# Kernel optimization log

Measured on AMD Instinct MI355X. Metric: run time of the kernel, lower is better.

The kernel has to match this reference:

```python
import jax, jax.numpy as jnp
import numpy as np

N, E, F_IN, HID = 50000, 800000, 64, 64
RADIAL = 16  # 4 coordinate channels -> 4x4 gram matrix


def _l2norm(x, eps=1e-12):
    # F.normalize(x, dim=-1, p=2)
    n = jnp.linalg.norm(x, axis=-1, keepdims=True)
    return x / jnp.maximum(n, eps)


def setup_inputs() -> dict:
    key = jax.random.key(0)
    ks = jax.random.split(key, 14)

    def lin(k, i, o, scale=None):
        s = (1.0 / np.sqrt(i)) if scale is None else scale
        return (jax.random.normal(k, (i, o), jnp.float32) * s).astype(jnp.float32)

    return dict(
        h=jax.random.normal(ks[0], (N, F_IN), jnp.float32),
        Z=jax.random.normal(ks[1], (N, 4, 3), jnp.float32),
        row=jax.random.randint(ks[2], (E,), 0, N),
        col=jax.random.randint(ks[3], (E,), 0, N),
        # edge_mlp: Linear(2*F_IN+16, HID) -> ReLU -> Linear(HID, HID) -> ReLU
        We1=lin(ks[4], 2 * F_IN + RADIAL, HID), be1=jnp.zeros((HID,), jnp.float32),
        We2=lin(ks[5], HID, HID), be2=jnp.zeros((HID,), jnp.float32),
        # node_mlp: Linear(HID+F_IN+HID, HID) -> ReLU -> Linear(HID, F_IN)
        Wn1=lin(ks[6], HID + F_IN + HID, HID), bn1=jnp.zeros((HID,), jnp.float32),
        Wn2=lin(ks[7], HID, F_IN), bn2=jnp.zeros((F_IN,), jnp.float32),
        # coord_mlp: Linear(HID, HID) -> ReLU -> Linear(HID, 1, bias=False, xavier gain 1e-3)
        Wc1=lin(ks[8], HID, HID), bc1=jnp.zeros((HID,), jnp.float32),
        Wc2=lin(ks[9], HID, 1, scale=0.001),
        # coord_mlp_vel: Linear(F_IN, HID) -> ReLU -> Linear(HID, 1)
        Wv1=lin(ks[10], F_IN, HID), bv1=jnp.zeros((HID,), jnp.float32),
        Wv2=lin(ks[11], HID, 1), bv2=jnp.zeros((1,), jnp.float32),
    )


def reference(h, Z, row, col, We1, be1, We2, be2, Wn1, bn1, Wn2, bn2,
              Wc1, bc1, Wc2, Wv1, bv1, Wv2, bv2):
    n = h.shape[0]
    # ---- coord2radial ----
    coord_diff = Z[row] - Z[col]                                 # [E,4,3]
    gram = jnp.einsum('ejt,ekt->ejk', coord_diff, coord_diff)    # [E,4,4]
    radial = _l2norm(gram.reshape(gram.shape[0], -1))            # [E,16]
    # ---- edge model ----
    e_in = jnp.concatenate([h[row], h[col], radial], axis=1)     # [E,144]
    edge_feat = jax.nn.relu(jax.nn.relu(e_in @ We1 + be1) @ We2 + be2)  # [E,HID]
    # ---- coord model (segment-mean over receiving node `row`) ----
    phi = jax.nn.relu(edge_feat @ Wc1 + bc1) @ Wc2               # [E,1]
    trans = coord_diff * phi[:, :, None]                         # [E,4,3]
    seg = jax.ops.segment_sum(trans, row, num_segments=n)        # [N,4,3]
    ones_e = jnp.ones((row.shape[0],), trans.dtype)
    cnt_row = jnp.maximum(jax.ops.segment_sum(ones_e, row, num_segments=n), 1.0)
    f = seg / cnt_row[:, None, None]                             # coords_weight = 1.0
    Z_new = Z + f                                                # [N,4,3]
    # ---- node model ----
    agg = jax.ops.segment_sum(edge_feat, row, num_segments=n)    # [N,HID]
    cnt_col = jnp.maximum(jax.ops.segment_sum(ones_e, col, num_segments=n), 1.0)
    others = jax.ops.segment_sum(edge_feat, col, num_segments=n) / cnt_col[:, None]
    n_in = jnp.concatenate([others, h, agg], axis=1)             # [N, HID+F_IN+HID]
    h_new = h + (jax.nn.relu(n_in @ Wn1 + bn1) @ Wn2 + bn2)      # recurrent
    # ---- Isolated update: x = Z[:,0], v = Z[:,1], force = f[:,0] ----
    scale = jax.nn.relu(h_new @ Wv1 + bv1) @ Wv2 + bv2           # [N,1]
    v_new = scale * Z[:, 1] + f[:, 0]                            # [N,3]
    x_new = Z[:, 0] + v_new                                      # [N,3]
    return (h_new, Z_new, x_new, v_new)
```

## Files before the change

kernel.cpp:

```cpp
#include <hip/hip_runtime.h>
#include <stdint.h>


__device__ __forceinline__ uint32_t bf16round(float x) {
    uint32_t u = __float_as_uint(x);
    return (u + 0x7fffu + ((u >> 16) & 1u)) >> 16;
}
__device__ __forceinline__ uint32_t packbf(float a, float b) {
    return bf16round(a) | (bf16round(b) << 16);
}
__device__ __forceinline__ float bflo(uint32_t u) { return __uint_as_float(u << 16); }
__device__ __forceinline__ float bfhi(uint32_t u) { return __uint_as_float(u & 0xffff0000u); }
__device__ __forceinline__ float bfu(ushort u) { return __uint_as_float(((uint32_t)u) << 16); }

typedef __attribute__((ext_vector_type(8))) short short8;
typedef __attribute__((ext_vector_type(4))) float f32x4;

__device__ __forceinline__ int wave_incl_scan(int x) {
    int lane = threadIdx.x & 63;
    #pragma unroll
    for (int off = 1; off < 64; off <<= 1) {
        int y = __shfl_up(x, off, 64);
        if (lane >= off) x += y;
    }
    return x;
}

__global__ __launch_bounds__(256) void hist_rank(
    const int* __restrict__ row, const int* __restrict__ col,
    int* __restrict__ cntR, int* __restrict__ cntC,
    int* __restrict__ rank_r, int* __restrict__ rank_c, int E)
{
    int i = blockIdx.x * blockDim.x + threadIdx.x;
    int stride = gridDim.x * blockDim.x;
    for (; i < E; i += stride) {
        rank_r[i] = atomicAdd(&cntR[row[i]], 1);
        rank_c[i] = atomicAdd(&cntC[col[i]], 1);
    }
}

__global__ __launch_bounds__(1024) void scan_block(
    const int* __restrict__ srcR, const int* __restrict__ srcC,
    int* __restrict__ dstR, int* __restrict__ dstC,
    int* __restrict__ bsumR, int* __restrict__ bsumC, int N)
{
    const int* src = blockIdx.y ? srcC : srcR;
    int* dst  = blockIdx.y ? dstC : dstR;
    int* bsum = blockIdx.y ? bsumC : bsumR;
    __shared__ int s[17];
    int tid = threadIdx.x, lane = tid & 63, wid = tid >> 6;
    int i = blockIdx.x * 1024 + tid;
    int x = (i < N) ? src[i] : 0;
    int incl = wave_incl_scan(x);
    if (lane == 63) s[wid] = incl;
    __syncthreads();
    if (wid == 0) {
        int t = (lane < 16) ? s[lane] : 0;
        int sc = t;
        #pragma unroll
        for (int off = 1; off < 16; off <<= 1) {
            int y = __shfl_up(sc, off, 64);
            if (lane >= off) sc += y;
        }
        if (lane < 16) s[lane] = sc - t;
        if (lane == 15) s[16] = sc;
    }
    __syncthreads();
    if (i < N) dst[i] = s[wid] + incl - x;
    if (tid == 0) bsum[blockIdx.x] = s[16];
}

__global__ __launch_bounds__(64) void scan_totals(
    int* __restrict__ bsumR, int* __restrict__ bsumC,
    int* __restrict__ dstR, int* __restrict__ dstC, int nblk, int N)
{
    int lane = threadIdx.x;
    for (int which = 0; which < 2; which++) {
        int* bs = which ? bsumC : bsumR;
        int* dst = which ? dstC : dstR;
        int running = 0;
        for (int base = 0; base < nblk; base += 64) {
            int idx = base + lane;
            int x = (idx < nblk) ? bs[idx] : 0;
            int incl = wave_incl_scan(x);
            if (idx < nblk) bs[idx] = running + incl - x;
            running += __shfl(incl, 63, 64);
        }
        if (lane == 0) dst[N] = running;
    }
}

__global__ __launch_bounds__(1024) void scan_add(
    int* __restrict__ dstR, int* __restrict__ dstC,
    const int* __restrict__ bsumR, const int* __restrict__ bsumC, int N)
{
    int* dst = blockIdx.y ? dstC : dstR;
    const int* bsum = blockIdx.y ? bsumC : bsumR;
    int i = blockIdx.x * 1024 + threadIdx.x;
    if (i < N) dst[i] += bsum[blockIdx.x];
}

__global__ __launch_bounds__(256) void perm_build(
    const int* __restrict__ row, const int* __restrict__ col,
    const int* __restrict__ rowptr, const int* __restrict__ colptr,
    const int* __restrict__ rank_r, const int* __restrict__ rank_c,
    int* __restrict__ rs_row, int* __restrict__ rs_col, int* __restrict__ rs_pc, int E)
{
    int i = blockIdx.x * blockDim.x + threadIdx.x;
    int stride = gridDim.x * blockDim.x;
    for (; i < E; i += stride) {
        int r = row[i], c = col[i];
        int pr = rowptr[r] + rank_r[i];
        int pc = colptr[c] + rank_c[i];
        rs_row[pr] = r;
        rs_col[pr] = c;
        rs_pc[pr]  = pc;
    }
}

__global__ __launch_bounds__(256) void precompute_xrowcol(
    const float* __restrict__ h, const float* __restrict__ We1,
    const float* __restrict__ be1,
    ushort* __restrict__ Xrow, ushort* __restrict__ Xcol,
    ushort* __restrict__ hbf, int N)
{
    __shared__ uint32_t sWa[32 * 64];
    __shared__ uint32_t sWb[32 * 64];
    __shared__ float sbe1[64];
    int tid = threadIdx.x;
    for (int idx = tid; idx < 32 * 64; idx += 256) {
        int p = idx >> 6, o = idx & 63;
        sWa[idx] = packbf(We1[(2 * p) * 64 + o],      We1[(2 * p + 1) * 64 + o]);
        sWb[idx] = packbf(We1[(64 + 2 * p) * 64 + o], We1[(64 + 2 * p + 1) * 64 + o]);
    }
    if (tid < 64) sbe1[tid] = be1[tid];
    __syncthreads();

    int lane = tid & 63;
    int wv = blockIdx.x * 4 + (tid >> 6);
    int nw = gridDim.x * 4;
    for (int n0 = wv; n0 < N; n0 += nw) {
        int n = __builtin_amdgcn_readfirstlane(n0);
        const float* hn = h + (size_t)n * 64;
        float acc1 = sbe1[lane], acc2 = 0.f;
        #pragma unroll 8
        for (int p = 0; p < 32; p++) {
            float a0 = hn[2 * p], a1 = hn[2 * p + 1];
            uint32_t wa = sWa[p * 64 + lane];
            uint32_t wb = sWb[p * 64 + lane];
            acc1 += a0 * bflo(wa) + a1 * bfhi(wa);
            acc2 += a0 * bflo(wb) + a1 * bfhi(wb);
        }
        Xrow[(size_t)n * 64 + lane] = (ushort)bf16round(acc1);
        Xcol[(size_t)n * 64 + lane] = (ushort)bf16round(acc2);
        hbf[(size_t)n * 64 + lane]  = (ushort)bf16round(hn[lane]);
    }
}

__global__ __launch_bounds__(256) void edge_kernel(
    const float* __restrict__ Z,
    const int* __restrict__ rs_row, const int* __restrict__ rs_col,
    const int* __restrict__ rs_pc,
    const ushort* __restrict__ Xrow, const ushort* __restrict__ Xcol,
    const float* __restrict__ We1, const float* __restrict__ We2, const float* __restrict__ be2,
    const float* __restrict__ Wc1, const float* __restrict__ bc1, const float* __restrict__ Wc2,
    ushort* __restrict__ ef_col,
    float* __restrict__ aggF, float* __restrict__ segF, int E)
{
    __shared__ ushort radT[4][16 * 32];
    __shared__ ushort h1T[4][16 * 72];
    __shared__ ushort efT[4][16 * 72];
    __shared__ ushort xrT[4][16 * 72];
    __shared__ float  cdT[4][16 * 12];
    __shared__ float  phiT[4][16];

    int tid   = threadIdx.x;
    int lane  = tid & 63;
    int wslot = tid >> 6;
    int l16   = lane & 15;
    int quad  = lane >> 4;

    short8 w1r[4], w2f0[4], w2f1[4], w3f0[4], w3f1[4];
    float be2v[4], bc1v[4], wc2v[4];
    #pragma unroll
    for (int nt = 0; nt < 4; nt++) {
        int n = nt * 16 + l16;
        #pragma unroll
        for (int j = 0; j < 8; j++) {
            int k = quad * 8 + j;
            w1r[nt][j]  = (k < 16) ? (short)bf16round(We1[(128 + k) * 64 + n]) : (short)0;
            w2f0[nt][j] = (short)bf16round(We2[k * 64 + n]);
            w2f1[nt][j] = (short)bf16round(We2[(32 + k) * 64 + n]);
            w3f0[nt][j] = (short)bf16round(Wc1[k * 64 + n]);
            w3f1[nt][j] = (short)bf16round(Wc1[(32 + k) * 64 + n]);
        }
        be2v[nt] = be2[n];
        bc1v[nt] = bc1[n];
        wc2v[nt] = Wc2[n];
    }

    {
        int e = lane >> 2, o = (lane & 3) * 4;
        *(uint2*)&radT[wslot][e * 32 + 16 + o] = make_uint2(0u, 0u);
    }

    int e_l = lane >> 2;
    int cb  = (lane & 3) * 3;

    const f32x4 z4 = {0.f, 0.f, 0.f, 0.f};
    int ntile = (E + 15) >> 4;
    for (int t = blockIdx.x * 4 + wslot; t < ntile; t += gridDim.x * 4) {
        int e0 = t * 16;
        int eidx = e0 + l16;
        int eclmp = min(eidx, E - 1);
        int rowv = rs_row[eclmp];
        int colv = rs_col[eclmp];
        int pcv  = rs_pc[eclmp];

        {
            int off = lane & 7, es = lane >> 3;
            #pragma unroll
            for (int i = 0; i < 2; i++) {
                int e = es + i * 8;
                int nr = __shfl(rowv, e, 64);
                int nc = __shfl(colv, e, 64);
                uint4 vr = *(const uint4*)(Xrow + (size_t)nr * 64 + off * 8);
                uint4 vc = *(const uint4*)(Xcol + (size_t)nc * 64 + off * 8);
                *(uint4*)&xrT[wslot][e * 72 + off * 8] = vr;
                *(uint4*)&efT[wslot][e * 72 + off * 8] = vc;
            }
        }

        int rZ = __shfl(rowv, e_l, 64);
        int cZ = __shfl(colv, e_l, 64);
        const float* Zr = Z + (size_t)rZ * 12 + cb;
        const float* Zc = Z + (size_t)cZ * 12 + cb;
        float cd0 = Zr[0] - Zc[0];
        float cd1 = Zr[1] - Zc[1];
        float cd2 = Zr[2] - Zc[2];
        cdT[wslot][e_l * 12 + cb + 0] = cd0;
        cdT[wslot][e_l * 12 + cb + 1] = cd1;
        cdT[wslot][e_l * 12 + cb + 2] = cd2;

        int gbase = lane & ~3;
        float g0, g1, g2, g3;
        {
            float a0 = __shfl(cd0, gbase + 0, 64), b0 = __shfl(cd1, gbase + 0, 64), c0 = __shfl(cd2, gbase + 0, 64);
            float a1 = __shfl(cd0, gbase + 1, 64), b1 = __shfl(cd1, gbase + 1, 64), c1 = __shfl(cd2, gbase + 1, 64);
            float a2 = __shfl(cd0, gbase + 2, 64), b2 = __shfl(cd1, gbase + 2, 64), c2 = __shfl(cd2, gbase + 2, 64);
            float a3 = __shfl(cd0, gbase + 3, 64), b3 = __shfl(cd1, gbase + 3, 64), c3 = __shfl(cd2, gbase + 3, 64);
            g0 = cd0 * a0 + cd1 * b0 + cd2 * c0;
            g1 = cd0 * a1 + cd1 * b1 + cd2 * c1;
            g2 = cd0 * a2 + cd1 * b2 + cd2 * c2;
            g3 = cd0 * a3 + cd1 * b3 + cd2 * c3;
        }
        float s = g0 * g0 + g1 * g1 + g2 * g2 + g3 * g3;
        s += __shfl_xor(s, 1, 64);
        s += __shfl_xor(s, 2, 64);
        float inv = 1.f / fmaxf(sqrtf(s), 1e-12f);

        __builtin_amdgcn_wave_barrier();
        uint2 rp;
        rp.x = packbf(g0 * inv, g1 * inv);
        rp.y = packbf(g2 * inv, g3 * inv);
        *(uint2*)&radT[wslot][e_l * 32 + (lane & 3) * 4] = rp;
        __builtin_amdgcn_wave_barrier();

        short8 aR = *(const short8*)&radT[wslot][l16 * 32 + quad * 8];
        f32x4 c1t[4];
        #pragma unroll
        for (int nt = 0; nt < 4; nt++)
            c1t[nt] = __builtin_amdgcn_mfma_f32_16x16x32_bf16(aR, w1r[nt], z4, 0, 0, 0);

        __builtin_amdgcn_wave_barrier();
        #pragma unroll
        for (int nt = 0; nt < 4; nt++) {
            int n = nt * 16 + l16;
            #pragma unroll
            for (int reg = 0; reg < 4; reg++) {
                int eL = quad * 4 + reg;
                float hv = c1t[nt][reg]
                         + bfu(xrT[wslot][eL * 72 + n])
                         + bfu(efT[wslot][eL * 72 + n]);
                hv = fmaxf(hv, 0.f);
                h1T[wslot][eL * 72 + n] = (ushort)bf16round(hv);
            }
        }
        __builtin_amdgcn_wave_barrier();

        short8 a20 = *(const short8*)&h1T[wslot][l16 * 72 + quad * 8];
        short8 a21 = *(const short8*)&h1T[wslot][l16 * 72 + 32 + quad * 8];
        f32x4 c2t[4];
        #pragma unroll
        for (int nt = 0; nt < 4; nt++) {
            f32x4 a = __builtin_amdgcn_mfma_f32_16x16x32_bf16(a20, w2f0[nt], z4, 0, 0, 0);
            c2t[nt]  = __builtin_amdgcn_mfma_f32_16x16x32_bf16(a21, w2f1[nt], a, 0, 0, 0);
        }

        __builtin_amdgcn_wave_barrier();
        #pragma unroll
        for (int nt = 0; nt < 4; nt++) {
            int n = nt * 16 + l16;
            #pragma unroll
            for (int reg = 0; reg < 4; reg++) {
                float ef = fmaxf(c2t[nt][reg] + be2v[nt], 0.f);
                efT[wslot][(quad * 4 + reg) * 72 + n] = (ushort)bf16round(ef);
            }
        }
        __builtin_amdgcn_wave_barrier();

        {
            int off = lane & 7, es = lane >> 3;
            #pragma unroll
            for (int i = 0; i < 2; i++) {
                int e = es + i * 8;
                int pc = __shfl(pcv, e, 64);
                if (e0 + e < E)
                    *(uint4*)(ef_col + (size_t)pc * 64 + off * 8) =
                        *(const uint4*)&efT[wslot][e * 72 + off * 8];
            }
        }

        short8 a30 = *(const short8*)&efT[wslot][l16 * 72 + quad * 8];
        short8 a31 = *(const short8*)&efT[wslot][l16 * 72 + 32 + quad * 8];
        float ps[4] = {0.f, 0.f, 0.f, 0.f};
        #pragma unroll
        for (int nt = 0; nt < 4; nt++) {
            f32x4 a = __builtin_amdgcn_mfma_f32_16x16x32_bf16(a30, w3f0[nt], z4, 0, 0, 0);
            f32x4 c = __builtin_amdgcn_mfma_f32_16x16x32_bf16(a31, w3f1[nt], a, 0, 0, 0);
            #pragma unroll
            for (int reg = 0; reg < 4; reg++)
                ps[reg] += fmaxf(c[reg] + bc1v[nt], 0.f) * wc2v[nt];
        }
        #pragma unroll
        for (int reg = 0; reg < 4; reg++) {
            ps[reg] += __shfl_xor(ps[reg], 1, 64);
            ps[reg] += __shfl_xor(ps[reg], 2, 64);
            ps[reg] += __shfl_xor(ps[reg], 4, 64);
            ps[reg] += __shfl_xor(ps[reg], 8, 64);
        }
        __builtin_amdgcn_wave_barrier();
        if (l16 == 0) {
            f32x4 pv = {ps[0], ps[1], ps[2], ps[3]};
            *(f32x4*)&phiT[wslot][quad * 4] = pv;
        }
        __builtin_amdgcn_wave_barrier();

        {
            int curnode = __shfl(rowv, 0, 64);
            int a = 0;
            float accA = 0.f, accS = 0.f;
            #pragma unroll
            for (int e = 0; e < 16; e++) {
                bool valid = (e0 + e) < E;
                float v = valid ? bfu(efT[wslot][e * 72 + lane]) : 0.f;
                float sv = 0.f;
                if (lane < 12 && valid)
                    sv = phiT[wslot][e] * cdT[wslot][e * 12 + lane];
                accA += v;
                accS += sv;
                int nxt = (e < 15) ? __shfl(rowv, e + 1, 64) : -1;
                if (nxt != curnode) {
                    if (a > 0 && e < 15) {
                        aggF[(size_t)curnode * 64 + lane] = accA;
                        if (lane < 12) segF[(size_t)curnode * 12 + lane] = accS;
                    } else if ((e0 + a) < E) {
                        unsafeAtomicAdd(&aggF[(size_t)curnode * 64 + lane], accA);
                        if (lane < 12) unsafeAtomicAdd(&segF[(size_t)curnode * 12 + lane], accS);
                    }
                    curnode = nxt;
                    a = e + 1;
                    accA = 0.f;
                    accS = 0.f;
                }
            }
        }
        __builtin_amdgcn_wave_barrier();
    }
}

__global__ __launch_bounds__(256) void reduce_kernel(
    const int* __restrict__ colptr, const ushort* __restrict__ ef_col,
    ushort* __restrict__ othersB, int N)
{
    int tid = threadIdx.x;
    int lane = tid & 63, wslot = tid >> 6;
    int wv = blockIdx.x * 4 + wslot, nw = gridDim.x * 4;

    for (int n0 = wv; n0 < N; n0 += nw) {
        int n = __builtin_amdgcn_readfirstlane(n0);
        int cs = colptr[n], ceN = colptr[n + 1];
        float inv_col = 1.f / (float)max(ceN - cs, 1);

        float othv = 0.f;
        int p = cs;
        for (; p + 1 < ceN; p += 2) {
            othv += bfu(ef_col[(size_t)p * 64 + lane])
                  + bfu(ef_col[(size_t)(p + 1) * 64 + lane]);
        }
        if (p < ceN) othv += bfu(ef_col[(size_t)p * 64 + lane]);
        othv *= inv_col;

        othersB[(size_t)n * 64 + lane] = (ushort)bf16round(othv);
    }
}

__global__ __launch_bounds__(256) void mlp_kernel(
    const float* __restrict__ h, const float* __restrict__ Z,
    const ushort* __restrict__ hbf,
    const float* __restrict__ aggF, const ushort* __restrict__ othersB,
    const float* __restrict__ segF, const int* __restrict__ rowptr,
    const float* __restrict__ Wn1, const float* __restrict__ bn1,
    const float* __restrict__ Wn2, const float* __restrict__ bn2,
    const float* __restrict__ Wv1, const float* __restrict__ bv1,
    const float* __restrict__ Wv2, const float* __restrict__ bv2,
    float* __restrict__ out, int N)
{
    __shared__ ushort aT[4][16 * 200];
    __shared__ ushort h1T[4][16 * 72];
    __shared__ float  scT[4][16];
    __shared__ float  irT[4][16];

    int tid   = threadIdx.x;
    int lane  = tid & 63;
    int wslot = tid >> 6;
    int l16   = lane & 15;
    int quad  = lane >> 4;

    short8 wn1f[6][4], wn2f[2][4], wv1f[2][4];
    float bn1v[4], bn2v[4], bv1v[4], wv2v[4];
    #pragma unroll
    for (int nt = 0; nt < 4; nt++) {
        int n = nt * 16 + l16;
        #pragma unroll
        for (int kc = 0; kc < 6; kc++)
            #pragma unroll
            for (int j = 0; j < 8; j++)
                wn1f[kc][nt][j] = (short)bf16round(Wn1[(kc * 32 + quad * 8 + j) * 64 + n]);
        #pragma unroll
        for (int kc = 0; kc < 2; kc++)
            #pragma unroll
            for (int j = 0; j < 8; j++) {
                wn2f[kc][nt][j] = (short)bf16round(Wn2[(kc * 32 + quad * 8 + j) * 64 + n]);
                wv1f[kc][nt][j] = (short)bf16round(Wv1[(kc * 32 + quad * 8 + j) * 64 + n]);
            }
        bn1v[nt] = bn1[n];
        bn2v[nt] = bn2[n];
        bv1v[nt] = bv1[n];
        wv2v[nt] = Wv2[n];
    }
    float bv2s = bv2[0];

    const f32x4 z4 = {0.f, 0.f, 0.f, 0.f};
    size_t OZ = (size_t)N * 64, OX = (size_t)N * 76, OV = (size_t)N * 79;
    int ntile = (N + 15) >> 4;
    for (int t = blockIdx.x * 4 + wslot; t < ntile; t += gridDim.x * 4) {
        int n0 = t * 16;

        if (lane < 16) {
            int node = min(n0 + lane, N - 1);
            irT[wslot][lane] = 1.f / (float)max(rowptr[node + 1] - rowptr[node], 1);
        }

        {
            #pragma unroll
            for (int i = 0; i < 2; i++) {
                int c = i * 64 + lane;
                int r = c >> 3, off = c & 7;
                int nn = min(n0 + r, N - 1);
                uint4 vo = *(const uint4*)(othersB + (size_t)nn * 64 + off * 8);
                uint4 vh = *(const uint4*)(hbf     + (size_t)nn * 64 + off * 8);
                float4 f0 = *(const float4*)(aggF + (size_t)nn * 64 + off * 8);
                float4 f1 = *(const float4*)(aggF + (size_t)nn * 64 + off * 8 + 4);
                uint4 va = make_uint4(packbf(f0.x, f0.y), packbf(f0.z, f0.w),
                                      packbf(f1.x, f1.y), packbf(f1.z, f1.w));
                *(uint4*)&aT[wslot][r * 200 +       off * 8] = vo;
                *(uint4*)&aT[wslot][r * 200 +  64 + off * 8] = vh;
                *(uint4*)&aT[wslot][r * 200 + 128 + off * 8] = va;
            }
        }
        __builtin_amdgcn_wave_barrier();

        #pragma unroll
        for (int i = 0; i < 4; i++) {
            int nd = i * 4 + (lane >> 4);
            int comp = lane & 15;
            int node = n0 + nd;
            if (comp < 12 && node < N) {
                float f = segF[(size_t)node * 12 + comp] * irT[wslot][nd];
                out[OZ + (size_t)node * 12 + comp] = Z[(size_t)node * 12 + comp] + f;
            }
        }

        f32x4 c1t[4];
        short8 af[6];
        #pragma unroll
        for (int kc = 0; kc < 6; kc++)
            af[kc] = *(const short8*)&aT[wslot][l16 * 200 + kc * 32 + quad * 8];
        #pragma unroll
        for (int nt = 0; nt < 4; nt++) {
            f32x4 c = z4;
            #pragma unroll
            for (int kc = 0; kc < 6; kc++)
                c = __builtin_amdgcn_mfma_f32_16x16x32_bf16(af[kc], wn1f[kc][nt], c, 0, 0, 0);
            c1t[nt] = c;
        }
        __builtin_amdgcn_wave_barrier();
        #pragma unroll
        for (int nt = 0; nt < 4; nt++) {
            int n = nt * 16 + l16;
            #pragma unroll
            for (int reg = 0; reg < 4; reg++) {
                float hv = fmaxf(c1t[nt][reg] + bn1v[nt], 0.f);
                h1T[wslot][(quad * 4 + reg) * 72 + n] = (ushort)bf16round(hv);
            }
        }
        __builtin_amdgcn_wave_barrier();

        short8 a20 = *(const short8*)&h1T[wslot][l16 * 72 + quad * 8];
        short8 a21 = *(const short8*)&h1T[wslot][l16 * 72 + 32 + quad * 8];
        f32x4 hnewT[4];
        #pragma unroll
        for (int nt = 0; nt < 4; nt++) {
            f32x4 a = __builtin_amdgcn_mfma_f32_16x16x32_bf16(a20, wn2f[0][nt], z4, 0, 0, 0);
            f32x4 c = __builtin_amdgcn_mfma_f32_16x16x32_bf16(a21, wn2f[1][nt], a, 0, 0, 0);
            int n = nt * 16 + l16;
            #pragma unroll
            for (int reg = 0; reg < 4; reg++) {
                int node = n0 + quad * 4 + reg;
                int nc = min(node, N - 1);
                float hnew = h[(size_t)nc * 64 + n] + c[reg] + bn2v[nt];
                hnewT[nt][reg] = hnew;
                if (node < N) out[(size_t)node * 64 + n] = hnew;
            }
        }

        __builtin_amdgcn_wave_barrier();
        #pragma unroll
        for (int nt = 0; nt < 4; nt++) {
            int n = nt * 16 + l16;
            #pragma unroll
            for (int reg = 0; reg < 4; reg++)
                h1T[wslot][(quad * 4 + reg) * 72 + n] = (ushort)bf16round(hnewT[nt][reg]);
        }
        __builtin_amdgcn_wave_barrier();
        short8 a30 = *(const short8*)&h1T[wslot][l16 * 72 + quad * 8];
        short8 a31 = *(const short8*)&h1T[wslot][l16 * 72 + 32 + quad * 8];
        float ps[4] = {0.f, 0.f, 0.f, 0.f};
        #pragma unroll
        for (int nt = 0; nt < 4; nt++) {
            f32x4 a = __builtin_amdgcn_mfma_f32_16x16x32_bf16(a30, wv1f[0][nt], z4, 0, 0, 0);
            f32x4 c = __builtin_amdgcn_mfma_f32_16x16x32_bf16(a31, wv1f[1][nt], a, 0, 0, 0);
            #pragma unroll
            for (int reg = 0; reg < 4; reg++)
                ps[reg] += fmaxf(c[reg] + bv1v[nt], 0.f) * wv2v[nt];
        }
        #pragma unroll
        for (int reg = 0; reg < 4; reg++) {
            ps[reg] += __shfl_xor(ps[reg], 1, 64);
            ps[reg] += __shfl_xor(ps[reg], 2, 64);
            ps[reg] += __shfl_xor(ps[reg], 4, 64);
            ps[reg] += __shfl_xor(ps[reg], 8, 64);
        }
        __builtin_amdgcn_wave_barrier();
        if (l16 == 0) {
            f32x4 pv = {ps[0] + bv2s, ps[1] + bv2s, ps[2] + bv2s, ps[3] + bv2s};
            *(f32x4*)&scT[wslot][quad * 4] = pv;
        }
        __builtin_amdgcn_wave_barrier();

        if (lane < 48) {
            int nd = lane / 3, comp = lane - nd * 3;
            int node = n0 + nd;
            if (node < N) {
                float scale = scT[wslot][nd];
                float f = segF[(size_t)node * 12 + comp] * irT[wslot][nd];
                float v = scale * Z[(size_t)node * 12 + 3 + comp] + f;
                float x = Z[(size_t)node * 12 + comp] + v;
                out[OX + (size_t)node * 3 + comp] = x;
                out[OV + (size_t)node * 3 + comp] = v;
            }
        }
        __builtin_amdgcn_wave_barrier();
    }
}

extern "C" void kernel_launch(void* const* d_in, const int* in_sizes, int n_in,
                              void* d_out, int out_size, void* d_ws, size_t ws_size,
                              hipStream_t stream) {
    const float* h   = (const float*)d_in[0];
    const float* Z   = (const float*)d_in[1];
    const int*   row = (const int*)d_in[2];
    const int*   col = (const int*)d_in[3];
    const float* We1 = (const float*)d_in[4];
    const float* be1 = (const float*)d_in[5];
    const float* We2 = (const float*)d_in[6];
    const float* be2 = (const float*)d_in[7];
    const float* Wn1 = (const float*)d_in[8];
    const float* bn1 = (const float*)d_in[9];
    const float* Wn2 = (const float*)d_in[10];
    const float* bn2 = (const float*)d_in[11];
    const float* Wc1 = (const float*)d_in[12];
    const float* bc1 = (const float*)d_in[13];
    const float* Wc2 = (const float*)d_in[14];
    const float* Wv1 = (const float*)d_in[15];
    const float* bv1 = (const float*)d_in[16];
    const float* Wv2 = (const float*)d_in[17];
    const float* bv2 = (const float*)d_in[18];

    int N = in_sizes[0] / 64;
    int E = in_sizes[2];
    int nblk = (N + 1023) / 1024;

    char* ws = (char*)d_ws;
    size_t o = 0;
    int* cntR    = (int*)(ws + o); o += (size_t)N * 4;
    int* cntC    = (int*)(ws + o); o += (size_t)N * 4;
    float* aggF  = (float*)(ws + o); o += (size_t)N * 64 * 4;
    float* segF  = (float*)(ws + o); o += (size_t)N * 12 * 4;
    size_t zero_bytes = o;
    int* rowptr  = (int*)(ws + o); o += (size_t)(N + 1) * 4;
    int* colptr  = (int*)(ws + o); o += (size_t)(N + 1) * 4;
    int* bsumR   = (int*)(ws + o); o += (size_t)nblk * 4;
    int* bsumC   = (int*)(ws + o); o += (size_t)nblk * 4;
    int* rank_r  = (int*)(ws + o); o += (size_t)E * 4;
    int* rank_c  = (int*)(ws + o); o += (size_t)E * 4;
    int* rs_row  = (int*)(ws + o); o += (size_t)E * 4;
    int* rs_col  = (int*)(ws + o); o += (size_t)E * 4;
    int* rs_pc   = (int*)(ws + o); o += (size_t)E * 4;
    ushort* Xrow = (ushort*)(ws + o); o += (size_t)N * 64 * 2;
    ushort* Xcol = (ushort*)(ws + o); o += (size_t)N * 64 * 2;
    ushort* hbf  = (ushort*)(ws + o); o += (size_t)N * 64 * 2;
    ushort* othersB = (ushort*)(ws + o); o += (size_t)N * 64 * 2;
    ushort* ef_col  = (ushort*)(ws + o); o += (size_t)E * 64 * 2;
    float* out = (float*)d_out;

    hipMemsetAsync(d_ws, 0, zero_bytes, stream);
    hist_rank<<<1024, 256, 0, stream>>>(row, col, cntR, cntC, rank_r, rank_c, E);
    scan_block<<<dim3(nblk, 2), 1024, 0, stream>>>(cntR, cntC, rowptr, colptr,
                                                   bsumR, bsumC, N);
    scan_totals<<<1, 64, 0, stream>>>(bsumR, bsumC, rowptr, colptr, nblk, N);
    scan_add<<<dim3(nblk, 2), 1024, 0, stream>>>(rowptr, colptr, bsumR, bsumC, N);
    perm_build<<<1024, 256, 0, stream>>>(row, col, rowptr, colptr,
                                         rank_r, rank_c, rs_row, rs_col, rs_pc, E);
    precompute_xrowcol<<<512, 256, 0, stream>>>(h, We1, be1, Xrow, Xcol, hbf, N);
    edge_kernel<<<1024, 256, 0, stream>>>(Z, rs_row, rs_col, rs_pc, Xrow, Xcol,
                                          We1, We2, be2, Wc1, bc1, Wc2,
                                          ef_col, aggF, segF, E);
    reduce_kernel<<<2048, 256, 0, stream>>>(colptr, ef_col, othersB, N);
    mlp_kernel<<<800, 256, 0, stream>>>(h, Z, hbf, aggF, othersB, segF, rowptr,
                                        Wn1, bn1, Wn2, bn2, Wv1, bv1, Wv2, bv2,
                                        out, N);
}
```

Measured before the change: 488.4 us.

## Fuse histogram with node precompute, fold col-reduction into MLP, stage weights in LDS

The histogram/rank kernel and the node-side We1 precompute now run in one launch, split by block index, so the two independent jobs overlap. The separate column-reduction kernel is removed. The MLP kernel now averages ef_col rows per node directly into its shared tile, which avoids writing and re-reading the othersB buffer. In the edge kernel the We1-radial and Wc1 MFMA operands move from registers to shared memory to reduce register pressure, at the cost of extra LDS reads per tile and an added block barrier.

```diff
diff --git a/kernel.cpp b/kernel.cpp
--- a/kernel.cpp
+++ b/kernel.cpp
@@ -26,16 +26,57 @@
     return x;
 }
 
-__global__ __launch_bounds__(256) void hist_rank(
+#define HIST_BLOCKS 640
+#define HP_GRID 1024
+__global__ __launch_bounds__(256) void hist_pre(
     const int* __restrict__ row, const int* __restrict__ col,
     int* __restrict__ cntR, int* __restrict__ cntC,
-    int* __restrict__ rank_r, int* __restrict__ rank_c, int E)
+    int* __restrict__ rank_r, int* __restrict__ rank_c, int E,
+    const float* __restrict__ h, const float* __restrict__ We1,
+    const float* __restrict__ be1,
+    ushort* __restrict__ Xrow, ushort* __restrict__ Xcol,
+    ushort* __restrict__ hbf, int N)
 {
-    int i = blockIdx.x * blockDim.x + threadIdx.x;
-    int stride = gridDim.x * blockDim.x;
-    for (; i < E; i += stride) {
-        rank_r[i] = atomicAdd(&cntR[row[i]], 1);
-        rank_c[i] = atomicAdd(&cntC[col[i]], 1);
+    __shared__ uint32_t sWa[32 * 64];
+    __shared__ uint32_t sWb[32 * 64];
+    __shared__ float sbe1[64];
+    int tid = threadIdx.x;
+
+    if (blockIdx.x < HIST_BLOCKS) {
+        int i = blockIdx.x * 256 + tid;
+        int stride = HIST_BLOCKS * 256;
+        for (; i < E; i += stride) {
+            rank_r[i] = atomicAdd(&cntR[row[i]], 1);
+            rank_c[i] = atomicAdd(&cntC[col[i]], 1);
+        }
+    } else {
+        for (int idx = tid; idx < 32 * 64; idx += 256) {
+            int p = idx >> 6, o = idx & 63;
+            sWa[idx] = packbf(We1[(2 * p) * 64 + o],      We1[(2 * p + 1) * 64 + o]);
+            sWb[idx] = packbf(We1[(64 + 2 * p) * 64 + o], We1[(64 + 2 * p + 1) * 64 + o]);
+        }
+        if (tid < 64) sbe1[tid] = be1[tid];
+        __syncthreads();
+
+        int lane = tid & 63;
+        int wv = (blockIdx.x - HIST_BLOCKS) * 4 + (tid >> 6);
+        int nw = (HP_GRID - HIST_BLOCKS) * 4;
+        for (int n0 = wv; n0 < N; n0 += nw) {
+            int n = __builtin_amdgcn_readfirstlane(n0);
+            const float* hn = h + (size_t)n * 64;
+            float acc1 = sbe1[lane], acc2 = 0.f;
+            #pragma unroll 8
+            for (int p = 0; p < 32; p++) {
+                float a0 = hn[2 * p], a1 = hn[2 * p + 1];
+                uint32_t wa = sWa[p * 64 + lane];
+                uint32_t wb = sWb[p * 64 + lane];
+                acc1 += a0 * bflo(wa) + a1 * bfhi(wa);
+                acc2 += a0 * bflo(wb) + a1 * bfhi(wb);
+            }
+            Xrow[(size_t)n * 64 + lane] = (ushort)bf16round(acc1);
+            Xcol[(size_t)n * 64 + lane] = (ushort)bf16round(acc2);
+            hbf[(size_t)n * 64 + lane]  = (ushort)bf16round(hn[lane]);
+        }
     }
 }
 
@@ -118,45 +159,6 @@
     }
 }
 
-__global__ __launch_bounds__(256) void precompute_xrowcol(
-    const float* __restrict__ h, const float* __restrict__ We1,
-    const float* __restrict__ be1,
-    ushort* __restrict__ Xrow, ushort* __restrict__ Xcol,
-    ushort* __restrict__ hbf, int N)
-{
-    __shared__ uint32_t sWa[32 * 64];
-    __shared__ uint32_t sWb[32 * 64];
-    __shared__ float sbe1[64];
-    int tid = threadIdx.x;
-    for (int idx = tid; idx < 32 * 64; idx += 256) {
-        int p = idx >> 6, o = idx & 63;
-        sWa[idx] = packbf(We1[(2 * p) * 64 + o],      We1[(2 * p + 1) * 64 + o]);
-        sWb[idx] = packbf(We1[(64 + 2 * p) * 64 + o], We1[(64 + 2 * p + 1) * 64 + o]);
-    }
-    if (tid < 64) sbe1[tid] = be1[tid];
-    __syncthreads();
-
-    int lane = tid & 63;
-    int wv = blockIdx.x * 4 + (tid >> 6);
-    int nw = gridDim.x * 4;
-    for (int n0 = wv; n0 < N; n0 += nw) {
-        int n = __builtin_amdgcn_readfirstlane(n0);
-        const float* hn = h + (size_t)n * 64;
-        float acc1 = sbe1[lane], acc2 = 0.f;
-        #pragma unroll 8
-        for (int p = 0; p < 32; p++) {
-            float a0 = hn[2 * p], a1 = hn[2 * p + 1];
-            uint32_t wa = sWa[p * 64 + lane];
-            uint32_t wb = sWb[p * 64 + lane];
-            acc1 += a0 * bflo(wa) + a1 * bfhi(wa);
-            acc2 += a0 * bflo(wb) + a1 * bfhi(wb);
-        }
-        Xrow[(size_t)n * 64 + lane] = (ushort)bf16round(acc1);
-        Xcol[(size_t)n * 64 + lane] = (ushort)bf16round(acc2);
-        hbf[(size_t)n * 64 + lane]  = (ushort)bf16round(hn[lane]);
-    }
-}
-
 __global__ __launch_bounds__(256) void edge_kernel(
     const float* __restrict__ Z,
     const int* __restrict__ rs_row, const int* __restrict__ rs_col,
@@ -173,6 +175,9 @@
     __shared__ ushort xrT[4][16 * 72];
     __shared__ float  cdT[4][16 * 12];
     __shared__ float  phiT[4][16];
+    __shared__ short w1rL[4 * 64 * 8];
+    __shared__ short w3aL[4 * 64 * 8];
+    __shared__ short w3bL[4 * 64 * 8];
 
     int tid   = threadIdx.x;
     int lane  = tid & 63;
@@ -180,7 +185,26 @@
     int l16   = lane & 15;
     int quad  = lane >> 4;
 
-    short8 w1r[4], w2f0[4], w2f1[4], w3f0[4], w3f1[4];
+    if (tid < 64) {
+        int tl16 = tid & 15, tquad = tid >> 4;
+        #pragma unroll
+        for (int nt = 0; nt < 4; nt++) {
+            int n = nt * 16 + tl16;
+            short8 v1, v3a, v3b;
+            #pragma unroll
+            for (int j = 0; j < 8; j++) {
+                int k = tquad * 8 + j;
+                v1[j]  = (k < 16) ? (short)bf16round(We1[(128 + k) * 64 + n]) : (short)0;
+                v3a[j] = (short)bf16round(Wc1[k * 64 + n]);
+                v3b[j] = (short)bf16round(Wc1[(32 + k) * 64 + n]);
+            }
+            *(short8*)&w1rL[(nt * 64 + tid) * 8] = v1;
+            *(short8*)&w3aL[(nt * 64 + tid) * 8] = v3a;
+            *(short8*)&w3bL[(nt * 64 + tid) * 8] = v3b;
+        }
+    }
+
+    short8 w2f0[4], w2f1[4];
     float be2v[4], bc1v[4], wc2v[4];
     #pragma unroll
     for (int nt = 0; nt < 4; nt++) {
@@ -188,11 +212,8 @@
         #pragma unroll
         for (int j = 0; j < 8; j++) {
             int k = quad * 8 + j;
-            w1r[nt][j]  = (k < 16) ? (short)bf16round(We1[(128 + k) * 64 + n]) : (short)0;
             w2f0[nt][j] = (short)bf16round(We2[k * 64 + n]);
             w2f1[nt][j] = (short)bf16round(We2[(32 + k) * 64 + n]);
-            w3f0[nt][j] = (short)bf16round(Wc1[k * 64 + n]);
-            w3f1[nt][j] = (short)bf16round(Wc1[(32 + k) * 64 + n]);
         }
         be2v[nt] = be2[n];
         bc1v[nt] = bc1[n];
@@ -203,6 +224,7 @@
         int e = lane >> 2, o = (lane & 3) * 4;
         *(uint2*)&radT[wslot][e * 32 + 16 + o] = make_uint2(0u, 0u);
     }
+    __syncthreads();
 
     int e_l = lane >> 2;
     int cb  = (lane & 3) * 3;
@@ -269,8 +291,10 @@
         short8 aR = *(const short8*)&radT[wslot][l16 * 32 + quad * 8];
         f32x4 c1t[4];
         #pragma unroll
-        for (int nt = 0; nt < 4; nt++)
-            c1t[nt] = __builtin_amdgcn_mfma_f32_16x16x32_bf16(aR, w1r[nt], z4, 0, 0, 0);
+        for (int nt = 0; nt < 4; nt++) {
+            short8 w1 = *(const short8*)&w1rL[(nt * 64 + lane) * 8];
+            c1t[nt] = __builtin_amdgcn_mfma_f32_16x16x32_bf16(aR, w1, z4, 0, 0, 0);
+        }
 
         __builtin_amdgcn_wave_barrier();
         #pragma unroll
@@ -326,8 +350,10 @@
         float ps[4] = {0.f, 0.f, 0.f, 0.f};
         #pragma unroll
         for (int nt = 0; nt < 4; nt++) {
-            f32x4 a = __builtin_amdgcn_mfma_f32_16x16x32_bf16(a30, w3f0[nt], z4, 0, 0, 0);
-            f32x4 c = __builtin_amdgcn_mfma_f32_16x16x32_bf16(a31, w3f1[nt], a, 0, 0, 0);
+            short8 w3a = *(const short8*)&w3aL[(nt * 64 + lane) * 8];
+            short8 w3b = *(const short8*)&w3bL[(nt * 64 + lane) * 8];
+            f32x4 a = __builtin_amdgcn_mfma_f32_16x16x32_bf16(a30, w3a, z4, 0, 0, 0);
+            f32x4 c = __builtin_amdgcn_mfma_f32_16x16x32_bf16(a31, w3b, a, 0, 0, 0);
             #pragma unroll
             for (int reg = 0; reg < 4; reg++)
                 ps[reg] += fmaxf(c[reg] + bc1v[nt], 0.f) * wc2v[nt];
@@ -379,36 +405,11 @@
     }
 }
 
-__global__ __launch_bounds__(256) void reduce_kernel(
-    const int* __restrict__ colptr, const ushort* __restrict__ ef_col,
-    ushort* __restrict__ othersB, int N)
-{
-    int tid = threadIdx.x;
-    int lane = tid & 63, wslot = tid >> 6;
-    int wv = blockIdx.x * 4 + wslot, nw = gridDim.x * 4;
-
-    for (int n0 = wv; n0 < N; n0 += nw) {
-        int n = __builtin_amdgcn_readfirstlane(n0);
-        int cs = colptr[n], ceN = colptr[n + 1];
-        float inv_col = 1.f / (float)max(ceN - cs, 1);
-
-        float othv = 0.f;
-        int p = cs;
-        for (; p + 1 < ceN; p += 2) {
-            othv += bfu(ef_col[(size_t)p * 64 + lane])
-                  + bfu(ef_col[(size_t)(p + 1) * 64 + lane]);
-        }
-        if (p < ceN) othv += bfu(ef_col[(size_t)p * 64 + lane]);
-        othv *= inv_col;
-
-        othersB[(size_t)n * 64 + lane] = (ushort)bf16round(othv);
-    }
-}
-
 __global__ __launch_bounds__(256) void mlp_kernel(
     const float* __restrict__ h, const float* __restrict__ Z,
     const ushort* __restrict__ hbf,
-    const float* __restrict__ aggF, const ushort* __restrict__ othersB,
+    const float* __restrict__ aggF,
+    const ushort* __restrict__ ef_col, const int* __restrict__ colptr,
     const float* __restrict__ segF, const int* __restrict__ rowptr,
     const float* __restrict__ Wn1, const float* __restrict__ bn1,
     const float* __restrict__ Wn2, const float* __restrict__ bn2,
@@ -463,18 +464,45 @@
         }
 
         {
+            int cp = 0;
+            if (lane < 17) cp = colptr[min(n0 + lane, N)];
+            int g  = lane >> 4;
+            int f4 = (lane & 15) * 4;
+            #pragma unroll 1
+            for (int nd = 0; nd < 16; nd++) {
+                int cs = __shfl(cp, nd, 64);
+                int ce = __shfl(cp, nd + 1, 64);
+                float f0 = 0.f, f1 = 0.f, f2 = 0.f, f3 = 0.f;
+                for (int p = cs + g; p < ce; p += 4) {
+                    uint2 v = *(const uint2*)(ef_col + (size_t)p * 64 + f4);
+                    f0 += bflo(v.x); f1 += bfhi(v.x);
+                    f2 += bflo(v.y); f3 += bfhi(v.y);
+                }
+                f0 += __shfl_xor(f0, 16, 64); f0 += __shfl_xor(f0, 32, 64);
+                f1 += __shfl_xor(f1, 16, 64); f1 += __shfl_xor(f1, 32, 64);
+                f2 += __shfl_xor(f2, 16, 64); f2 += __shfl_xor(f2, 32, 64);
+                f3 += __shfl_xor(f3, 16, 64); f3 += __shfl_xor(f3, 32, 64);
+                if (lane < 16) {
+                    float ic = 1.f / (float)max(ce - cs, 1);
+                    uint2 pk;
+                    pk.x = packbf(f0 * ic, f1 * ic);
+                    pk.y = packbf(f2 * ic, f3 * ic);
+                    *(uint2*)&aT[wslot][nd * 200 + f4] = pk;
+                }
+            }
+        }
+
+        {
             #pragma unroll
             for (int i = 0; i < 2; i++) {
                 int c = i * 64 + lane;
                 int r = c >> 3, off = c & 7;
                 int nn = min(n0 + r, N - 1);
-                uint4 vo = *(const uint4*)(othersB + (size_t)nn * 64 + off * 8);
-                uint4 vh = *(const uint4*)(hbf     + (size_t)nn * 64 + off * 8);
+                uint4 vh = *(const uint4*)(hbf + (size_t)nn * 64 + off * 8);
                 float4 f0 = *(const float4*)(aggF + (size_t)nn * 64 + off * 8);
                 float4 f1 = *(const float4*)(aggF + (size_t)nn * 64 + off * 8 + 4);
                 uint4 va = make_uint4(packbf(f0.x, f0.y), packbf(f0.z, f0.w),
                                       packbf(f1.x, f1.y), packbf(f1.z, f1.w));
-                *(uint4*)&aT[wslot][r * 200 +       off * 8] = vo;
                 *(uint4*)&aT[wslot][r * 200 +  64 + off * 8] = vh;
                 *(uint4*)&aT[wslot][r * 200 + 128 + off * 8] = va;
             }
@@ -631,24 +659,23 @@
     ushort* Xrow = (ushort*)(ws + o); o += (size_t)N * 64 * 2;
     ushort* Xcol = (ushort*)(ws + o); o += (size_t)N * 64 * 2;
     ushort* hbf  = (ushort*)(ws + o); o += (size_t)N * 64 * 2;
-    ushort* othersB = (ushort*)(ws + o); o += (size_t)N * 64 * 2;
-    ushort* ef_col  = (ushort*)(ws + o); o += (size_t)E * 64 * 2;
+    ushort* ef_col = (ushort*)(ws + o); o += (size_t)E * 64 * 2;
     float* out = (float*)d_out;
 
     hipMemsetAsync(d_ws, 0, zero_bytes, stream);
-    hist_rank<<<1024, 256, 0, stream>>>(row, col, cntR, cntC, rank_r, rank_c, E);
+    hist_pre<<<HP_GRID, 256, 0, stream>>>(row, col, cntR, cntC, rank_r, rank_c, E,
+                                          h, We1, be1, Xrow, Xcol, hbf, N);
     scan_block<<<dim3(nblk, 2), 1024, 0, stream>>>(cntR, cntC, rowptr, colptr,
                                                    bsumR, bsumC, N);
     scan_totals<<<1, 64, 0, stream>>>(bsumR, bsumC, rowptr, colptr, nblk, N);
     scan_add<<<dim3(nblk, 2), 1024, 0, stream>>>(rowptr, colptr, bsumR, bsumC, N);
     perm_build<<<1024, 256, 0, stream>>>(row, col, rowptr, colptr,
                                          rank_r, rank_c, rs_row, rs_col, rs_pc, E);
-    precompute_xrowcol<<<512, 256, 0, stream>>>(h, We1, be1, Xrow, Xcol, hbf, N);
     edge_kernel<<<1024, 256, 0, stream>>>(Z, rs_row, rs_col, rs_pc, Xrow, Xcol,
                                           We1, We2, be2, Wc1, bc1, Wc2,
                                           ef_col, aggF, segF, E);
-    reduce_kernel<<<2048, 256, 0, stream>>>(colptr, ef_col, othersB, N);
-    mlp_kernel<<<800, 256, 0, stream>>>(h, Z, hbf, aggF, othersB, segF, rowptr,
+    mlp_kernel<<<800, 256, 0, stream>>>(h, Z, hbf, aggF, ef_col, colptr,
+                                        segF, rowptr,
                                         Wn1, bn1, Wn2, bn2, Wv1, bv1, Wv2, bv2,
                                         out, N);
 }
```

Result: slower. 558.2 us (+14.3%).
